# Optimization experiments

Hardware: AMD Instinct MI355X
Metric: run time of the kernel (lower is better)

Reference implementation:

```python
import jax, jax.numpy as jnp
import numpy as np

B, T, C = 2, 2048, 1024
R = 16
LORA_SCALE = 1.0 / R  # lora_alpha(=1) / r


def lora_linear(x, w, b, a, bb):
    # loralib: y = x @ W^T + bias + (x @ A^T) @ B^T * scaling
    return x @ w.T + b + (x @ a.T) @ bb.T * LORA_SCALE


def setup_inputs() -> dict:
    key = jax.random.key(0)
    ks = jax.random.split(key, 8)
    s = 0.02
    return {
        "x": jax.random.normal(ks[0], (B, T, C), jnp.float32),
        "w_attn": jax.random.normal(ks[1], (3 * C, C), jnp.float32) * s,
        "b_attn": jnp.zeros((3 * C,), jnp.float32),
        "lora_a_attn": jax.random.normal(ks[2], (R, C), jnp.float32) * s,
        "lora_b_attn": jnp.zeros((3 * C, R), jnp.float32),
        "w_proj": jax.random.normal(ks[3], (C, C), jnp.float32) * s,
        "b_proj": jnp.zeros((C,), jnp.float32),
        "lora_a_proj": jax.random.normal(ks[4], (R, C), jnp.float32) * s,
        "lora_b_proj": jnp.zeros((C, R), jnp.float32),
        "n_head": 16,
    }


def reference(x, w_attn, b_attn, lora_a_attn, lora_b_attn, w_proj, b_proj,
              lora_a_proj, lora_b_proj, n_head):
    b, t, c = x.shape
    hd = c // n_head
    qkv = lora_linear(x, w_attn, b_attn, lora_a_attn, lora_b_attn)
    q, k, v = jnp.split(qkv, 3, axis=2)
    # (B, H, T, hd)
    q = q.reshape(b, t, n_head, hd).transpose(0, 2, 1, 3)
    k = k.reshape(b, t, n_head, hd).transpose(0, 2, 1, 3)
    v = v.reshape(b, t, n_head, hd).transpose(0, 2, 1, 3)
    att = jnp.einsum("bhqd,bhkd->bhqk", q, k) * (1.0 / np.sqrt(hd).astype(np.float32))
    causal = jnp.tril(jnp.ones((t, t), bool))
    att = jnp.where(causal[None, None], att, jnp.float32(-jnp.inf))
    att = jax.nn.softmax(att, axis=-1)
    y = jnp.einsum("bhqk,bhkd->bhqd", att, v)
    y = y.transpose(0, 2, 1, 3).reshape(b, t, c)
    return lora_linear(y, w_proj, b_proj, lora_a_proj, lora_b_proj)
```

## Files before the change

kernel.cpp:

```cpp
#include <hip/hip_runtime.h>

typedef __attribute__((ext_vector_type(8))) short bf16x8;
typedef __attribute__((ext_vector_type(4))) short bf16x4;
typedef __attribute__((ext_vector_type(4))) float f32x4;

__device__ __forceinline__ float bf2f(unsigned short u) {
    unsigned int x = ((unsigned int)u) << 16;
    float f;
    __builtin_memcpy(&f, &x, 4);
    return f;
}
__device__ __forceinline__ unsigned short f2bf(float f) {
    unsigned int x;
    __builtin_memcpy(&x, &f, 4);
    x += 0x7FFFu + ((x >> 16) & 1u);
    return (unsigned short)(x >> 16);
}

#define GLOAD_LDS16(gp, lp)                                      \
    __builtin_amdgcn_global_load_lds(                            \
        (const __attribute__((address_space(1))) void*)(gp),     \
        (__attribute__((address_space(3))) void*)(lp), 16, 0, 0)

__global__ __launch_bounds__(256) void prep(
    const float* __restrict__ x, unsigned short* __restrict__ xb,
    const float* __restrict__ w_attn, const float* __restrict__ la_attn,
    const float* __restrict__ lb_attn, unsigned short* __restrict__ Weff_attn,
    const float* __restrict__ w_proj, const float* __restrict__ la_proj,
    const float* __restrict__ lb_proj, unsigned short* __restrict__ Weff_proj) {
    const int bid = blockIdx.x;
    if (bid < 4096) {
        int i = (bid * 256 + threadIdx.x) * 4;
        float4 v = *(const float4*)(x + i);
        xb[i + 0] = f2bf(v.x);
        xb[i + 1] = f2bf(v.y);
        xb[i + 2] = f2bf(v.z);
        xb[i + 3] = f2bf(v.w);
        return;
    }
    const float* W;
    const float* Ain;
    const float* Bin;
    unsigned short* Weff;
    int idx;
    if (bid < 16384) {
        idx = (bid - 4096) * 256 + threadIdx.x;
        W = w_attn; Ain = la_attn; Bin = lb_attn; Weff = Weff_attn;
    } else {
        idx = (bid - 16384) * 256 + threadIdx.x;
        W = w_proj; Ain = la_proj; Bin = lb_proj; Weff = Weff_proj;
    }
    int n = idx >> 10;
    int k = idx & 1023;
    float s = 0.f;
#pragma unroll
    for (int r = 0; r < 16; ++r)
        s += Bin[n * 16 + r] * Ain[r * 1024 + k];
    Weff[idx] = f2bf(W[idx] + 0.0625f * s);
}

template <bool F32OUT, bool VSPLIT>
__global__ __launch_bounds__(256) void gemm_bt_bias(
    const unsigned short* __restrict__ A, const unsigned short* __restrict__ B,
    const float* __restrict__ bias, unsigned short* __restrict__ Cb,
    float* __restrict__ Cf, unsigned short* __restrict__ Vtout,
    int M, int N, int K) {
    __shared__ unsigned short sA[128 * 32];
    __shared__ unsigned short sB[128 * 32];
    const int tid = threadIdx.x;
    const int wave = tid >> 6, lane = tid & 63;
    const int quad = lane >> 4, l16 = lane & 15;
    const int m0 = blockIdx.y * 128, n0 = blockIdx.x * 128;
    const int wm = (wave & 1) * 64, wn = (wave >> 1) * 64;

    const int srow = wave * 32 + (lane >> 2);
    const int scol = (lane & 3) * 8;
    const unsigned short* Ag = A + (size_t)(m0 + srow) * K + scol;
    const unsigned short* Bg = B + (size_t)(n0 + srow) * K + scol;
    unsigned short* sAw = sA + wave * 1024;
    unsigned short* sBw = sB + wave * 1024;
    const size_t kjump = (size_t)16 * K;

    f32x4 acc[4][4];
#pragma unroll
    for (int i = 0; i < 4; ++i)
#pragma unroll
        for (int j = 0; j < 4; ++j) acc[i][j] = (f32x4){0.f, 0.f, 0.f, 0.f};

    for (int k0 = 0; k0 < K; k0 += 32) {
        __syncthreads();
        GLOAD_LDS16(Ag + k0, sAw);
        GLOAD_LDS16(Ag + k0 + kjump, sAw + 512);
        GLOAD_LDS16(Bg + k0, sBw);
        GLOAD_LDS16(Bg + k0 + kjump, sBw + 512);
        __syncthreads();
        bf16x8 af[4], bfr[4];
#pragma unroll
        for (int mi = 0; mi < 4; ++mi)
            af[mi] = *(const bf16x8*)&sA[(wm + mi * 16 + l16) * 32 + quad * 8];
#pragma unroll
        for (int ni = 0; ni < 4; ++ni)
            bfr[ni] = *(const bf16x8*)&sB[(wn + ni * 16 + l16) * 32 + quad * 8];
#pragma unroll
        for (int mi = 0; mi < 4; ++mi)
#pragma unroll
            for (int ni = 0; ni < 4; ++ni)
                acc[mi][ni] = __builtin_amdgcn_mfma_f32_16x16x32_bf16(
                    af[mi], bfr[ni], acc[mi][ni], 0, 0, 0);
    }
    float bv[4];
#pragma unroll
    for (int ni = 0; ni < 4; ++ni) bv[ni] = bias[n0 + wn + ni * 16 + l16];

    if (VSPLIT && n0 >= 2048) {
#pragma unroll
        for (int ni = 0; ni < 4; ++ni) {
            const int hcol = n0 + wn + ni * 16 + l16 - 2048;
#pragma unroll
            for (int mi = 0; mi < 4; ++mi) {
                const int rowtop = m0 + wm + mi * 16 + quad * 4;
                const int bb = rowtop >> 11;
                const int t = rowtop & 2047;
                bf16x4 pk;
#pragma unroll
                for (int r = 0; r < 4; ++r)
                    pk[r] = (short)f2bf(acc[mi][ni][r] + bv[ni]);
                *(bf16x4*)(Vtout +
                           ((size_t)((bb * 16 + (hcol >> 6)) * 64 + (hcol & 63))) *
                               2048 +
                           t) = pk;
            }
        }
        return;
    }

#pragma unroll
    for (int mi = 0; mi < 4; ++mi)
#pragma unroll
        for (int ni = 0; ni < 4; ++ni)
#pragma unroll
            for (int r = 0; r < 4; ++r) {
                int row = m0 + wm + mi * 16 + quad * 4 + r;
                int col = n0 + wn + ni * 16 + l16;
                float val = acc[mi][ni][r] + bv[ni];
                if (F32OUT)
                    Cf[(size_t)row * N + col] = val;
                else
                    Cb[(size_t)row * N + col] = f2bf(val);
            }
}

__global__ __launch_bounds__(256) void gemm_bt_bias64(
    const unsigned short* __restrict__ A, const unsigned short* __restrict__ B,
    const float* __restrict__ bias, float* __restrict__ Cf,
    int M, int N, int K) {
    __shared__ unsigned short sA[64 * 32];
    __shared__ unsigned short sB[128 * 32];
    const int tid = threadIdx.x;
    const int wave = tid >> 6, lane = tid & 63;
    const int quad = lane >> 4, l16 = lane & 15;
    const int m0 = blockIdx.y * 64, n0 = blockIdx.x * 128;
    const int wn = wave * 32;

    const int srowA = wave * 16 + (lane >> 2);
    const int srowB = wave * 32 + (lane >> 2);
    const int scol = (lane & 3) * 8;
    const unsigned short* Ag = A + (size_t)(m0 + srowA) * K + scol;
    const unsigned short* Bg = B + (size_t)(n0 + srowB) * K + scol;
    unsigned short* sAw = sA + wave * 512;
    unsigned short* sBw = sB + wave * 1024;
    const size_t kjump = (size_t)16 * K;

    f32x4 acc[4][2];
#pragma unroll
    for (int i = 0; i < 4; ++i)
#pragma unroll
        for (int j = 0; j < 2; ++j) acc[i][j] = (f32x4){0.f, 0.f, 0.f, 0.f};

    for (int k0 = 0; k0 < K; k0 += 32) {
        __syncthreads();
        GLOAD_LDS16(Ag + k0, sAw);
        GLOAD_LDS16(Bg + k0, sBw);
        GLOAD_LDS16(Bg + k0 + kjump, sBw + 512);
        __syncthreads();
        bf16x8 af[4], bfr[2];
#pragma unroll
        for (int mi = 0; mi < 4; ++mi)
            af[mi] = *(const bf16x8*)&sA[(mi * 16 + l16) * 32 + quad * 8];
#pragma unroll
        for (int ni = 0; ni < 2; ++ni)
            bfr[ni] = *(const bf16x8*)&sB[(wn + ni * 16 + l16) * 32 + quad * 8];
#pragma unroll
        for (int mi = 0; mi < 4; ++mi)
#pragma unroll
            for (int ni = 0; ni < 2; ++ni)
                acc[mi][ni] = __builtin_amdgcn_mfma_f32_16x16x32_bf16(
                    af[mi], bfr[ni], acc[mi][ni], 0, 0, 0);
    }
    float bv[2];
#pragma unroll
    for (int ni = 0; ni < 2; ++ni) bv[ni] = bias[n0 + wn + ni * 16 + l16];
#pragma unroll
    for (int mi = 0; mi < 4; ++mi)
#pragma unroll
        for (int ni = 0; ni < 2; ++ni)
#pragma unroll
            for (int r = 0; r < 4; ++r) {
                int row = m0 + mi * 16 + quad * 4 + r;
                int col = n0 + wn + ni * 16 + l16;
                Cf[(size_t)row * N + col] = acc[mi][ni][r] + bv[ni];
            }
}

__global__ __launch_bounds__(256) void attn_kernel(
    const unsigned short* __restrict__ qkv,
    const unsigned short* __restrict__ Vt,
    unsigned short* __restrict__ y) {
    const int b = blockIdx.z, h = blockIdx.y;
    const int bh = b * 16 + h;
    const int qblk = (int)blockIdx.x ^ (((bh >> 3) & 1) ? 31 : 0);
    const int w = threadIdx.x >> 6, lane = threadIdx.x & 63;
    const int quad = lane >> 4, l16 = lane & 15;
    const int q0 = qblk * 64 + w * 16;
    const int ntiles = qblk + 1;

    __shared__ unsigned short sK[64 * 72];
    __shared__ unsigned short sV[64 * 72];
    __shared__ unsigned short sP[4][16 * 72];

    const unsigned short* Qb = qkv + (size_t)(b * 2048) * 3072 + h * 64;
    const unsigned short* Kg = Qb + 1024;
    const unsigned short* Vg = Vt + (size_t)(bh * 64) * 2048;

    const int rlo = threadIdx.x >> 3;
    const int c8 = (threadIdx.x & 7) * 8;

    bf16x8 qf0 = *(const bf16x8*)(Qb + (size_t)(q0 + l16) * 3072 + quad * 8);
    bf16x8 qf1 = *(const bf16x8*)(Qb + (size_t)(q0 + l16) * 3072 + 32 + quad * 8);

    f32x4 o[4];
    float lacc = 0.f;
#pragma unroll
    for (int nt = 0; nt < 4; ++nt) o[nt] = (f32x4){0.f, 0.f, 0.f, 0.f};

    const float csc = 0.125f * 1.44269504088896340736f;

    bf16x8 kr0 = *(const bf16x8*)(Kg + (size_t)rlo * 3072 + c8);
    bf16x8 kr1 = *(const bf16x8*)(Kg + (size_t)(rlo + 32) * 3072 + c8);
    bf16x8 vr0 = *(const bf16x8*)(Vg + (size_t)rlo * 2048 + c8);
    bf16x8 vr1 = *(const bf16x8*)(Vg + (size_t)(rlo + 32) * 2048 + c8);

    for (int it = 0; it < ntiles; ++it) {
        const int kv0 = it * 64;
        __syncthreads();
        *(bf16x8*)&sK[rlo * 72 + c8] = kr0;
        *(bf16x8*)&sK[(rlo + 32) * 72 + c8] = kr1;
        *(bf16x8*)&sV[rlo * 72 + c8] = vr0;
        *(bf16x8*)&sV[(rlo + 32) * 72 + c8] = vr1;
        __syncthreads();
        if (it + 1 < ntiles) {
            const int nx = kv0 + 64;
            kr0 = *(const bf16x8*)(Kg + (size_t)(nx + rlo) * 3072 + c8);
            kr1 = *(const bf16x8*)(Kg + (size_t)(nx + rlo + 32) * 3072 + c8);
            vr0 = *(const bf16x8*)(Vg + (size_t)rlo * 2048 + nx + c8);
            vr1 = *(const bf16x8*)(Vg + (size_t)(rlo + 32) * 2048 + nx + c8);
        }

        f32x4 S[4];
#pragma unroll
        for (int f = 0; f < 4; ++f) {
            bf16x8 klo = *(const bf16x8*)&sK[(f * 16 + l16) * 72 + quad * 8];
            bf16x8 khi = *(const bf16x8*)&sK[(f * 16 + l16) * 72 + 32 + quad * 8];
            S[f] = (f32x4){0.f, 0.f, 0.f, 0.f};
            S[f] = __builtin_amdgcn_mfma_f32_16x16x32_bf16(klo, qf0, S[f], 0, 0, 0);
            S[f] = __builtin_amdgcn_mfma_f32_16x16x32_bf16(khi, qf1, S[f], 0, 0, 0);
        }
        const bool diag = (it == qblk);
        const int qr16 = w * 16 + l16;
#pragma unroll
        for (int f = 0; f < 4; ++f) {
            float p0, p1, p2, p3;
            {
                float sv = S[f][0] * csc;
                asm("v_exp_f32 %0, %1" : "=v"(p0) : "v"(sv));
                sv = S[f][1] * csc;
                asm("v_exp_f32 %0, %1" : "=v"(p1) : "v"(sv));
                sv = S[f][2] * csc;
                asm("v_exp_f32 %0, %1" : "=v"(p2) : "v"(sv));
                sv = S[f][3] * csc;
                asm("v_exp_f32 %0, %1" : "=v"(p3) : "v"(sv));
            }
            if (diag) {
                int c = f * 16 + quad * 4;
                p0 = (c + 0 <= qr16) ? p0 : 0.f;
                p1 = (c + 1 <= qr16) ? p1 : 0.f;
                p2 = (c + 2 <= qr16) ? p2 : 0.f;
                p3 = (c + 3 <= qr16) ? p3 : 0.f;
            }
            lacc += (p0 + p1) + (p2 + p3);
            unsigned int d0, d1;
            asm("v_cvt_pk_bf16_f32 %0, %1, %2" : "=v"(d0) : "v"(p0), "v"(p1));
            asm("v_cvt_pk_bf16_f32 %0, %1, %2" : "=v"(d1) : "v"(p2), "v"(p3));
            *(uint2*)&sP[w][l16 * 72 + f * 16 + quad * 4] = (uint2){d0, d1};
        }
        asm volatile("" ::: "memory");
        bf16x8 pf0 = *(const bf16x8*)&sP[w][l16 * 72 + quad * 8];
        bf16x8 pf1 = *(const bf16x8*)&sP[w][l16 * 72 + 32 + quad * 8];
#pragma unroll
        for (int nt = 0; nt < 4; ++nt) {
            bf16x8 v0 = *(const bf16x8*)&sV[(nt * 16 + l16) * 72 + quad * 8];
            bf16x8 v1 = *(const bf16x8*)&sV[(nt * 16 + l16) * 72 + 32 + quad * 8];
            o[nt] = __builtin_amdgcn_mfma_f32_16x16x32_bf16(pf0, v0, o[nt], 0, 0, 0);
            o[nt] = __builtin_amdgcn_mfma_f32_16x16x32_bf16(pf1, v1, o[nt], 0, 0, 0);
        }
    }

    lacc += __shfl_xor(lacc, 16);
    lacc += __shfl_xor(lacc, 32);
    float lt[4];
#pragma unroll
    for (int r = 0; r < 4; ++r) lt[r] = __shfl(lacc, quad * 4 + r);

    unsigned short* yb = y + (size_t)(b * 2048) * 1024 + h * 64;
#pragma unroll
    for (int nt = 0; nt < 4; ++nt)
#pragma unroll
        for (int r = 0; r < 4; ++r)
            yb[(size_t)(q0 + quad * 4 + r) * 1024 + nt * 16 + l16] =
                f2bf(o[nt][r] / lt[r]);
}

extern "C" void kernel_launch(void* const* d_in, const int* in_sizes, int n_in,
                              void* d_out, int out_size, void* d_ws, size_t ws_size,
                              hipStream_t stream) {
    const float* x       = (const float*)d_in[0];
    const float* w_attn  = (const float*)d_in[1];
    const float* b_attn  = (const float*)d_in[2];
    const float* la_attn = (const float*)d_in[3];
    const float* lb_attn = (const float*)d_in[4];
    const float* w_proj  = (const float*)d_in[5];
    const float* b_proj  = (const float*)d_in[6];
    const float* la_proj = (const float*)d_in[7];
    const float* lb_proj = (const float*)d_in[8];
    float* out = (float*)d_out;

    char* w = (char*)d_ws;
    unsigned short* xb        = (unsigned short*)w; w += (size_t)4096 * 1024 * 2;
    unsigned short* Weff_attn = (unsigned short*)w; w += (size_t)3072 * 1024 * 2;
    unsigned short* Weff_proj = (unsigned short*)w; w += (size_t)1024 * 1024 * 2;
    unsigned short* qkv       = (unsigned short*)w; w += (size_t)4096 * 3072 * 2;
    unsigned short* Vt        = (unsigned short*)w; w += (size_t)32 * 64 * 2048 * 2;
    unsigned short* y         = (unsigned short*)w; w += (size_t)4096 * 1024 * 2;

    prep<<<20480, 256, 0, stream>>>(x, xb, w_attn, la_attn, lb_attn, Weff_attn,
                                    w_proj, la_proj, lb_proj, Weff_proj);
    gemm_bt_bias<false, true><<<dim3(24, 32), 256, 0, stream>>>(
        xb, Weff_attn, b_attn, qkv, (float*)nullptr, Vt, 4096, 3072, 1024);
    attn_kernel<<<dim3(32, 16, 2), 256, 0, stream>>>(qkv, Vt, y);
    gemm_bt_bias64<<<dim3(8, 64), 256, 0, stream>>>(
        y, Weff_proj, b_proj, out, 4096, 1024, 1024);
}
```

Measured before the change: 203.2 us.

## Process 128 query rows per attention block, two 16-row tiles per wave

Each attention workgroup now covers 128 query rows instead of 64, with every wave computing two 16-row query tiles that share the same K/V tiles loaded into LDS. The grid is halved and the block-reversal swizzle now depends on batch index. This halves K/V global loads and LDS staging per query row and doubles MFMA work per barrier. The cost is more registers per wave, fewer blocks (512) to balance causal work, and coarser diagonal masking, where two tiles need masking and some fully masked work is still computed.

Result: slower. 210.2 us (+3.4%).

```diff
diff --git a/kernel.cpp b/kernel.cpp
--- a/kernel.cpp
+++ b/kernel.cpp
@@ -218,15 +218,16 @@
     unsigned short* __restrict__ y) {
     const int b = blockIdx.z, h = blockIdx.y;
     const int bh = b * 16 + h;
-    const int qblk = (int)blockIdx.x ^ (((bh >> 3) & 1) ? 31 : 0);
+    const int qblk = (int)blockIdx.x ^ (b ? 15 : 0);
     const int w = threadIdx.x >> 6, lane = threadIdx.x & 63;
     const int quad = lane >> 4, l16 = lane & 15;
-    const int q0 = qblk * 64 + w * 16;
-    const int ntiles = qblk + 1;
+    const int qA = qblk * 128 + w * 32;
+    const int qB = qA + 16;
+    const int ntiles = 2 * qblk + 2;
 
     __shared__ unsigned short sK[64 * 72];
     __shared__ unsigned short sV[64 * 72];
-    __shared__ unsigned short sP[4][16 * 72];
+    __shared__ unsigned short sP[4][32 * 72];
 
     const unsigned short* Qb = qkv + (size_t)(b * 2048) * 3072 + h * 64;
     const unsigned short* Kg = Qb + 1024;
@@ -235,13 +236,18 @@
     const int rlo = threadIdx.x >> 3;
     const int c8 = (threadIdx.x & 7) * 8;
 
-    bf16x8 qf0 = *(const bf16x8*)(Qb + (size_t)(q0 + l16) * 3072 + quad * 8);
-    bf16x8 qf1 = *(const bf16x8*)(Qb + (size_t)(q0 + l16) * 3072 + 32 + quad * 8);
-
-    f32x4 o[4];
-    float lacc = 0.f;
-#pragma unroll
-    for (int nt = 0; nt < 4; ++nt) o[nt] = (f32x4){0.f, 0.f, 0.f, 0.f};
+    bf16x8 qa0 = *(const bf16x8*)(Qb + (size_t)(qA + l16) * 3072 + quad * 8);
+    bf16x8 qa1 = *(const bf16x8*)(Qb + (size_t)(qA + l16) * 3072 + 32 + quad * 8);
+    bf16x8 qb0 = *(const bf16x8*)(Qb + (size_t)(qB + l16) * 3072 + quad * 8);
+    bf16x8 qb1 = *(const bf16x8*)(Qb + (size_t)(qB + l16) * 3072 + 32 + quad * 8);
+
+    f32x4 oA[4], oB[4];
+    float laccA = 0.f, laccB = 0.f;
+#pragma unroll
+    for (int nt = 0; nt < 4; ++nt) {
+        oA[nt] = (f32x4){0.f, 0.f, 0.f, 0.f};
+        oB[nt] = (f32x4){0.f, 0.f, 0.f, 0.f};
+    }
 
     const float csc = 0.125f * 1.44269504088896340736f;
 
@@ -266,68 +272,90 @@
             vr1 = *(const bf16x8*)(Vg + (size_t)(rlo + 32) * 2048 + nx + c8);
         }
 
-        f32x4 S[4];
+        f32x4 SA[4], SB[4];
 #pragma unroll
         for (int f = 0; f < 4; ++f) {
             bf16x8 klo = *(const bf16x8*)&sK[(f * 16 + l16) * 72 + quad * 8];
             bf16x8 khi = *(const bf16x8*)&sK[(f * 16 + l16) * 72 + 32 + quad * 8];
-            S[f] = (f32x4){0.f, 0.f, 0.f, 0.f};
-            S[f] = __builtin_amdgcn_mfma_f32_16x16x32_bf16(klo, qf0, S[f], 0, 0, 0);
-            S[f] = __builtin_amdgcn_mfma_f32_16x16x32_bf16(khi, qf1, S[f], 0, 0, 0);
-        }
-        const bool diag = (it == qblk);
-        const int qr16 = w * 16 + l16;
-#pragma unroll
-        for (int f = 0; f < 4; ++f) {
-            float p0, p1, p2, p3;
-            {
-                float sv = S[f][0] * csc;
-                asm("v_exp_f32 %0, %1" : "=v"(p0) : "v"(sv));
-                sv = S[f][1] * csc;
-                asm("v_exp_f32 %0, %1" : "=v"(p1) : "v"(sv));
-                sv = S[f][2] * csc;
-                asm("v_exp_f32 %0, %1" : "=v"(p2) : "v"(sv));
-                sv = S[f][3] * csc;
-                asm("v_exp_f32 %0, %1" : "=v"(p3) : "v"(sv));
+            SA[f] = (f32x4){0.f, 0.f, 0.f, 0.f};
+            SA[f] = __builtin_amdgcn_mfma_f32_16x16x32_bf16(klo, qa0, SA[f], 0, 0, 0);
+            SA[f] = __builtin_amdgcn_mfma_f32_16x16x32_bf16(khi, qa1, SA[f], 0, 0, 0);
+            SB[f] = (f32x4){0.f, 0.f, 0.f, 0.f};
+            SB[f] = __builtin_amdgcn_mfma_f32_16x16x32_bf16(klo, qb0, SB[f], 0, 0, 0);
+            SB[f] = __builtin_amdgcn_mfma_f32_16x16x32_bf16(khi, qb1, SB[f], 0, 0, 0);
+        }
+        const bool diag = (it >= 2 * qblk);
+#pragma unroll
+        for (int X = 0; X < 2; ++X) {
+            const int qr = (X ? qB : qA) + l16;
+            const int rowbase = X ? 16 : 0;
+            float* lp = X ? &laccB : &laccA;
+#pragma unroll
+            for (int f = 0; f < 4; ++f) {
+                f32x4 Sf = X ? SB[f] : SA[f];
+                float p0, p1, p2, p3;
+                {
+                    float sv = Sf[0] * csc;
+                    asm("v_exp_f32 %0, %1" : "=v"(p0) : "v"(sv));
+                    sv = Sf[1] * csc;
+                    asm("v_exp_f32 %0, %1" : "=v"(p1) : "v"(sv));
+                    sv = Sf[2] * csc;
+                    asm("v_exp_f32 %0, %1" : "=v"(p2) : "v"(sv));
+                    sv = Sf[3] * csc;
+                    asm("v_exp_f32 %0, %1" : "=v"(p3) : "v"(sv));
+                }
+                if (diag) {
+                    int c = kv0 + f * 16 + quad * 4;
+                    p0 = (c + 0 <= qr) ? p0 : 0.f;
+                    p1 = (c + 1 <= qr) ? p1 : 0.f;
+                    p2 = (c + 2 <= qr) ? p2 : 0.f;
+                    p3 = (c + 3 <= qr) ? p3 : 0.f;
+                }
+                *lp += (p0 + p1) + (p2 + p3);
+                unsigned int d0, d1;
+                asm("v_cvt_pk_bf16_f32 %0, %1, %2" : "=v"(d0) : "v"(p0), "v"(p1));
+                asm("v_cvt_pk_bf16_f32 %0, %1, %2" : "=v"(d1) : "v"(p2), "v"(p3));
+                *(uint2*)&sP[w][(rowbase + l16) * 72 + f * 16 + quad * 4] =
+                    (uint2){d0, d1};
             }
-            if (diag) {
-                int c = f * 16 + quad * 4;
-                p0 = (c + 0 <= qr16) ? p0 : 0.f;
-                p1 = (c + 1 <= qr16) ? p1 : 0.f;
-                p2 = (c + 2 <= qr16) ? p2 : 0.f;
-                p3 = (c + 3 <= qr16) ? p3 : 0.f;
-            }
-            lacc += (p0 + p1) + (p2 + p3);
-            unsigned int d0, d1;
-            asm("v_cvt_pk_bf16_f32 %0, %1, %2" : "=v"(d0) : "v"(p0), "v"(p1));
-            asm("v_cvt_pk_bf16_f32 %0, %1, %2" : "=v"(d1) : "v"(p2), "v"(p3));
-            *(uint2*)&sP[w][l16 * 72 + f * 16 + quad * 4] = (uint2){d0, d1};
         }
         asm volatile("" ::: "memory");
-        bf16x8 pf0 = *(const bf16x8*)&sP[w][l16 * 72 + quad * 8];
-        bf16x8 pf1 = *(const bf16x8*)&sP[w][l16 * 72 + 32 + quad * 8];
+        bf16x8 pfA0 = *(const bf16x8*)&sP[w][l16 * 72 + quad * 8];
+        bf16x8 pfA1 = *(const bf16x8*)&sP[w][l16 * 72 + 32 + quad * 8];
+        bf16x8 pfB0 = *(const bf16x8*)&sP[w][(16 + l16) * 72 + quad * 8];
+        bf16x8 pfB1 = *(const bf16x8*)&sP[w][(16 + l16) * 72 + 32 + quad * 8];
 #pragma unroll
         for (int nt = 0; nt < 4; ++nt) {
             bf16x8 v0 = *(const bf16x8*)&sV[(nt * 16 + l16) * 72 + quad * 8];
             bf16x8 v1 = *(const bf16x8*)&sV[(nt * 16 + l16) * 72 + 32 + quad * 8];
-            o[nt] = __builtin_amdgcn_mfma_f32_16x16x32_bf16(pf0, v0, o[nt], 0, 0, 0);
-            o[nt] = __builtin_amdgcn_mfma_f32_16x16x32_bf16(pf1, v1, o[nt], 0, 0, 0);
-        }
-    }
-
-    lacc += __shfl_xor(lacc, 16);
-    lacc += __shfl_xor(lacc, 32);
-    float lt[4];
-#pragma unroll
-    for (int r = 0; r < 4; ++r) lt[r] = __shfl(lacc, quad * 4 + r);
+            oA[nt] = __builtin_amdgcn_mfma_f32_16x16x32_bf16(pfA0, v0, oA[nt], 0, 0, 0);
+            oA[nt] = __builtin_amdgcn_mfma_f32_16x16x32_bf16(pfA1, v1, oA[nt], 0, 0, 0);
+            oB[nt] = __builtin_amdgcn_mfma_f32_16x16x32_bf16(pfB0, v0, oB[nt], 0, 0, 0);
+            oB[nt] = __builtin_amdgcn_mfma_f32_16x16x32_bf16(pfB1, v1, oB[nt], 0, 0, 0);
+        }
+    }
+
+    laccA += __shfl_xor(laccA, 16);
+    laccA += __shfl_xor(laccA, 32);
+    laccB += __shfl_xor(laccB, 16);
+    laccB += __shfl_xor(laccB, 32);
+    float ltA[4], ltB[4];
+#pragma unroll
+    for (int r = 0; r < 4; ++r) {
+        ltA[r] = __shfl(laccA, quad * 4 + r);
+        ltB[r] = __shfl(laccB, quad * 4 + r);
+    }
 
     unsigned short* yb = y + (size_t)(b * 2048) * 1024 + h * 64;
 #pragma unroll
     for (int nt = 0; nt < 4; ++nt)
 #pragma unroll
-        for (int r = 0; r < 4; ++r)
-            yb[(size_t)(q0 + quad * 4 + r) * 1024 + nt * 16 + l16] =
-                f2bf(o[nt][r] / lt[r]);
+        for (int r = 0; r < 4; ++r) {
+            yb[(size_t)(qA + quad * 4 + r) * 1024 + nt * 16 + l16] =
+                f2bf(oA[nt][r] / ltA[r]);
+            yb[(size_t)(qB + quad * 4 + r) * 1024 + nt * 16 + l16] =
+                f2bf(oB[nt][r] / ltB[r]);
+        }
 }
 
 extern "C" void kernel_launch(void* const* d_in, const int* in_sizes, int n_in,
@@ -356,7 +384,7 @@
                                     w_proj, la_proj, lb_proj, Weff_proj);
     gemm_bt_bias<false, true><<<dim3(24, 32), 256, 0, stream>>>(
         xb, Weff_attn, b_attn, qkv, (float*)nullptr, Vt, 4096, 3072, 1024);
-    attn_kernel<<<dim3(32, 16, 2), 256, 0, stream>>>(qkv, Vt, y);
+    attn_kernel<<<dim3(16, 16, 2), 256, 0, stream>>>(qkv, Vt, y);
     gemm_bt_bias64<<<dim3(8, 64), 256, 0, stream>>>(
         y, Weff_proj, b_proj, out, 4096, 1024, 1024);
 }
```
